# Kernel optimization log

Hardware: AMD Instinct MI355X
Metric: run time of the kernel (lower is better)

Reference implementation:

```python
import jax, jax.numpy as jnp
import numpy as np

N_NODES = 128   # input_series_dim (nodes per graph)
FEAT = 512      # input_series_length
HID = 512       # hidden_channels
OUT = 10        # output_dimension
BATCH = 512     # batch_size


def setup_inputs() -> dict:
    key = jax.random.key(0)
    ks = jax.random.split(key, 9)
    s = 0.02
    x = jax.random.normal(ks[0], (BATCH, N_NODES, FEAT), jnp.float32)
    # dense_to_sparse(ones(N_NODES, N_NODES)) -> fully connected incl. diagonal,
    # row-major order, covering only nodes 0..N_NODES-1 (faithful to source).
    r = jnp.repeat(jnp.arange(N_NODES, dtype=jnp.int32), N_NODES)
    c = jnp.tile(jnp.arange(N_NODES, dtype=jnp.int32), N_NODES)
    edge_index = jnp.stack([r, c])  # (2, N_NODES**2)
    batch = jnp.repeat(jnp.arange(BATCH, dtype=jnp.int32), N_NODES)  # (BATCH*N_NODES,)
    W1 = jax.random.normal(ks[1], (FEAT, HID), jnp.float32) * s
    b1 = jnp.zeros((HID,), jnp.float32)
    W2 = jax.random.normal(ks[2], (HID, HID), jnp.float32) * s
    b2 = jnp.zeros((HID,), jnp.float32)
    W3 = jax.random.normal(ks[3], (HID, HID), jnp.float32) * s
    b3 = jnp.zeros((HID,), jnp.float32)
    Wlin = jax.random.normal(ks[4], (HID, OUT), jnp.float32) * s
    blin = jnp.zeros((OUT,), jnp.float32)
    return {"x": x, "W1": W1, "b1": b1, "W2": W2, "b2": b2, "W3": W3,
            "b3": b3, "Wlin": Wlin, "blin": blin,
            "edge_index": edge_index, "batch": batch}


def gcn_conv(h, src, dst, W, b):
    # PyG GCNConv: linear transform, add self-loops for ALL N nodes, symmetric norm,
    # scatter-add aggregate at dst, add bias.
    N = h.shape[0]
    h = h @ W
    loop = jnp.arange(N, dtype=src.dtype)
    s = jnp.concatenate([src, loop])
    d = jnp.concatenate([dst, loop])
    deg = jax.ops.segment_sum(jnp.ones(s.shape[0], h.dtype), d, num_segments=N)
    dinv = jnp.where(deg > 0, jax.lax.rsqrt(deg), jnp.zeros((), h.dtype))
    norm = dinv[s] * dinv[d]                     # (E+N,)
    out = jax.ops.segment_sum(norm[:, None] * h[s], d, num_segments=N)
    return out + b


def reference(x, W1, b1, W2, b2, W3, b3, Wlin, blin, edge_index, batch):
    x = x.reshape(-1, x.shape[-1]).astype(jnp.float32)   # (B*N_NODES, FEAT)
    src, dst = edge_index[0], edge_index[1]
    h = jax.nn.relu(gcn_conv(x, src, dst, W1, b1))
    h = jax.nn.relu(gcn_conv(h, src, dst, W2, b2))
    h = gcn_conv(h, src, dst, W3, b3)                    # layers == 3 path
    B = BATCH
    sums = jax.ops.segment_sum(h, batch, num_segments=B)
    cnt = jax.ops.segment_sum(jnp.ones((h.shape[0],), h.dtype), batch, num_segments=B)
    pooled = sums / cnt[:, None]                         # global_mean_pool
    # dropout p=0.5 is identity in eval mode
    return pooled @ Wlin + blin                          # (BATCH, OUT)
```

## Files before the change

kernel.cpp:

```cpp
#include <hip/hip_runtime.h>
#include <hip/hip_bf16.h>


typedef __attribute__((ext_vector_type(8))) short short8;
typedef __attribute__((ext_vector_type(4))) float f32x4;
typedef __attribute__((ext_vector_type(2))) unsigned int uint2v;

#define AS_G __attribute__((address_space(1)))
#define AS_L __attribute__((address_space(3)))

__device__ __forceinline__ void gload_lds16(const void* g, void* l) {
  __builtin_amdgcn_global_load_lds((const AS_G void*)g, (AS_L void*)l, 16, 0, 0);
}

__device__ __forceinline__ unsigned int pack2_bf16(float a, float b) {
  unsigned int ua = __float_as_uint(a);
  unsigned int ub = __float_as_uint(b);
  ua += 0x7FFFu + ((ua >> 16) & 1u);
  ub += 0x7FFFu + ((ub >> 16) & 1u);
  return (ua >> 16) | (ub & 0xFFFF0000u);
}

__device__ __forceinline__ unsigned short bf16_rne(float a) {
  unsigned int ua = __float_as_uint(a);
  ua += 0x7FFFu + ((ua >> 16) & 1u);
  return (unsigned short)(ua >> 16);
}

__global__ __launch_bounds__(1024) void fused_gcn(
    const float* __restrict__ x,
    const __hip_bfloat16* __restrict__ W1t,
    const __hip_bfloat16* __restrict__ W2t,
    const float* __restrict__ b1,
    const float* __restrict__ b2,
    float* __restrict__ P)
{
  __shared__ __align__(16) __hip_bfloat16 smem[81920];

  const int t  = threadIdx.x;
  const int g  = blockIdx.x;
  const int wave = t >> 6;
  const int l    = t & 63;
  const int q    = l >> 4;
  const int r16  = l & 15;
  const int wm   = (wave & 1) * 64;
  const int wn   = (wave >> 1) * 64;

  const int arow = t >> 3;
  const int kq   = t & 7;
  const float* ga = x + ((size_t)g * 128 + arow) * 512 + kq * 4;
  const int awoff = arow * 32 + (((kq >> 1) ^ ((arow >> 1) & 3)) << 3) + (kq & 1) * 4;

  const int brow = t >> 2;
  const int bgc  = (t & 3) ^ ((brow >> 1) & 3);
  const size_t boff = (size_t)brow * 512 + bgc * 8;
  const __hip_bfloat16* g1b0 = W1t + boff;
  const __hip_bfloat16* g1b1 = g1b0 + (size_t)256 * 512;

  f32x4 acc[4][4];
#pragma unroll
  for (int i = 0; i < 4; ++i)
#pragma unroll
    for (int j = 0; j < 4; ++j)
      acc[i][j] = (f32x4)0.0f;

  {
    f32x4 a0 = *(const f32x4*)(const void*)ga;
    gload_lds16(g1b0, smem + 49152 + wave * 512);
    gload_lds16(g1b1, smem + 49152 + 8192 + wave * 512);
    uint2v w;
    w[0] = pack2_bf16(a0[0], a0[1]);
    w[1] = pack2_bf16(a0[2], a0[3]);
    *(uint2v*)(void*)(smem + awoff) = w;
  }
  for (int kt = 0; kt < 16; ++kt) {
    const int cur = kt & 1;
    const int nxt = cur ^ 1;
    __syncthreads();

    f32x4 aN;
    if (kt < 15) {
      const int ko = (kt + 1) * 32;
      aN = *(const f32x4*)(const void*)(ga + ko);
      gload_lds16(g1b0 + ko, smem + 49152 + nxt * 16384 + wave * 512);
      gload_lds16(g1b1 + ko, smem + 49152 + nxt * 16384 + 8192 + wave * 512);
    }

    short8 af[4], bfr[4];
#pragma unroll
    for (int i = 0; i < 4; ++i) {
      const int row = wm + i * 16 + r16;
      const int c   = (q ^ ((row >> 1) & 3)) << 3;
      af[i] = *(const short8*)(const void*)(smem + cur * 4096 + row * 32 + c);
    }
#pragma unroll
    for (int j = 0; j < 4; ++j) {
      const int row = wn + j * 16 + r16;
      const int c   = (q ^ ((row >> 1) & 3)) << 3;
      bfr[j] = *(const short8*)(const void*)(smem + 49152 + cur * 16384 + row * 32 + c);
    }
#pragma unroll
    for (int i = 0; i < 4; ++i)
#pragma unroll
      for (int j = 0; j < 4; ++j)
        acc[i][j] = __builtin_amdgcn_mfma_f32_16x16x32_bf16(af[i], bfr[j], acc[i][j], 0, 0, 0);

    if (kt < 15) {
      uint2v w;
      w[0] = pack2_bf16(aN[0], aN[1]);
      w[1] = pack2_bf16(aN[2], aN[3]);
      *(uint2v*)(void*)(smem + nxt * 4096 + awoff) = w;
    }
  }
  __syncthreads();

  float* redf = (float*)(smem + 65536);
  float* Sbuf = (float*)(smem + 67584);

  if (g == 0) {
    float sj[4];
#pragma unroll
    for (int j = 0; j < 4; ++j) {
      float a = 0.0f;
#pragma unroll
      for (int i = 0; i < 4; ++i)
#pragma unroll
        for (int r = 0; r < 4; ++r)
          a += acc[i][j][r];
      a += __shfl_xor(a, 16, 64);
      a += __shfl_xor(a, 32, 64);
      sj[j] = a;
    }
    if (q == 0) {
#pragma unroll
      for (int j = 0; j < 4; ++j) redf[wave * 64 + j * 16 + r16] = sj[j];
    }
    __syncthreads();
    if (t < 512)
      Sbuf[t] = redf[((t >> 6) * 2) * 64 + (t & 63)] +
                redf[((t >> 6) * 2 + 1) * 64 + (t & 63)];
    __syncthreads();
#pragma unroll
    for (int j = 0; j < 4; ++j) {
      const int col = wn + j * 16 + r16;
      const float bv = b1[col];
      const float Sv = Sbuf[col];
#pragma unroll
      for (int i = 0; i < 4; ++i)
#pragma unroll
        for (int r = 0; r < 4; ++r) {
          const int row = wm + i * 16 + q * 4 + r;
          const float v = fmaxf((Sv + acc[i][j][r]) * (1.0f / 129.0f) + bv, 0.0f);
          const float o = __shfl_xor(v, 1, 64);
          if ((r16 & 1) == 0) {
            const int sl = (col >> 3) ^ (row & 7);
            *(unsigned int*)(void*)(smem + row * 512 + sl * 8 + (col & 7)) = pack2_bf16(v, o);
          }
        }
    }
  } else {
#pragma unroll
    for (int j = 0; j < 4; ++j) {
      const int col = wn + j * 16 + r16;
      const float bv = b1[col];
#pragma unroll
      for (int i = 0; i < 4; ++i)
#pragma unroll
        for (int r = 0; r < 4; ++r) {
          const int row = wm + i * 16 + q * 4 + r;
          const float v = fmaxf(acc[i][j][r] + bv, 0.0f);
          const float o = __shfl_xor(v, 1, 64);
          if ((r16 & 1) == 0) {
            const int sl = (col >> 3) ^ (row & 7);
            *(unsigned int*)(void*)(smem + row * 512 + sl * 8 + (col & 7)) = pack2_bf16(v, o);
          }
        }
    }
  }

#pragma unroll
  for (int i = 0; i < 4; ++i)
#pragma unroll
    for (int j = 0; j < 4; ++j)
      acc[i][j] = (f32x4)0.0f;

  const __hip_bfloat16* g2b0 = W2t + boff;
  const __hip_bfloat16* g2b1 = g2b0 + (size_t)256 * 512;

  for (int kt = 0; kt < 16; ++kt) {
    __syncthreads();
    const int ko = kt * 32;
    gload_lds16(g2b0 + ko, smem + 65536 + wave * 512);
    gload_lds16(g2b1 + ko, smem + 65536 + 8192 + wave * 512);
    __syncthreads();

    short8 af[4], bfr[4];
#pragma unroll
    for (int i = 0; i < 4; ++i) {
      const int row = wm + i * 16 + r16;
      const int sl  = (kt * 4 + q) ^ (row & 7);
      af[i] = *(const short8*)(const void*)(smem + row * 512 + sl * 8);
    }
#pragma unroll
    for (int j = 0; j < 4; ++j) {
      const int row = wn + j * 16 + r16;
      const int c   = (q ^ ((row >> 1) & 3)) << 3;
      bfr[j] = *(const short8*)(const void*)(smem + 65536 + row * 32 + c);
    }
#pragma unroll
    for (int i = 0; i < 4; ++i)
#pragma unroll
      for (int j = 0; j < 4; ++j)
        acc[i][j] = __builtin_amdgcn_mfma_f32_16x16x32_bf16(af[i], bfr[j], acc[i][j], 0, 0, 0);
  }
  __syncthreads();

  float pj[4];
  if (g == 0) {
    float sj[4];
#pragma unroll
    for (int j = 0; j < 4; ++j) {
      float a = 0.0f;
#pragma unroll
      for (int i = 0; i < 4; ++i)
#pragma unroll
        for (int r = 0; r < 4; ++r)
          a += acc[i][j][r];
      a += __shfl_xor(a, 16, 64);
      a += __shfl_xor(a, 32, 64);
      sj[j] = a;
    }
    if (q == 0) {
#pragma unroll
      for (int j = 0; j < 4; ++j) redf[wave * 64 + j * 16 + r16] = sj[j];
    }
    __syncthreads();
    if (t < 512)
      Sbuf[t] = redf[((t >> 6) * 2) * 64 + (t & 63)] +
                redf[((t >> 6) * 2 + 1) * 64 + (t & 63)];
    __syncthreads();
#pragma unroll
    for (int j = 0; j < 4; ++j) {
      const float bv = b2[wn + j * 16 + r16];
      const float Sv = Sbuf[wn + j * 16 + r16];
      float a = 0.0f;
#pragma unroll
      for (int i = 0; i < 4; ++i)
#pragma unroll
        for (int r = 0; r < 4; ++r)
          a += fmaxf((Sv + acc[i][j][r]) * (1.0f / 129.0f) + bv, 0.0f);
      a += __shfl_xor(a, 16, 64);
      a += __shfl_xor(a, 32, 64);
      pj[j] = a;
    }
  } else {
#pragma unroll
    for (int j = 0; j < 4; ++j) {
      const float bv = b2[wn + j * 16 + r16];
      float a = 0.0f;
#pragma unroll
      for (int i = 0; i < 4; ++i)
#pragma unroll
        for (int r = 0; r < 4; ++r)
          a += fmaxf(acc[i][j][r] + bv, 0.0f);
      a += __shfl_xor(a, 16, 64);
      a += __shfl_xor(a, 32, 64);
      pj[j] = a;
    }
  }
  if (q == 0) {
#pragma unroll
    for (int j = 0; j < 4; ++j) redf[wave * 64 + j * 16 + r16] = pj[j];
  }
  __syncthreads();
  if (t < 512)
    P[(size_t)g * 512 + t] =
        (redf[((t >> 6) * 2) * 64 + (t & 63)] +
         redf[((t >> 6) * 2 + 1) * 64 + (t & 63)]) * (1.0f / 128.0f);
}

__global__ void fold_w(const float* __restrict__ W3,
                       const float* __restrict__ Wlin,
                       const float* __restrict__ b3,
                       const float* __restrict__ blin,
                       float* __restrict__ Wf, float* __restrict__ bfv) {
  const int c = blockIdx.x;
  const int l = threadIdx.x;
  float acc[10];
#pragma unroll
  for (int o = 0; o < 10; ++o) acc[o] = 0.0f;
  for (int n = l; n < 512; n += 64) {
    const float wv = W3[c * 512 + n];
#pragma unroll
    for (int o = 0; o < 10; ++o) acc[o] += wv * Wlin[n * 10 + o];
  }
#pragma unroll
  for (int off = 32; off; off >>= 1)
#pragma unroll
    for (int o = 0; o < 10; ++o) acc[o] += __shfl_down(acc[o], off, 64);
  if (l == 0) {
#pragma unroll
    for (int o = 0; o < 10; ++o) Wf[c * 10 + o] = acc[o];
  }
  if (c < 10) {
    float s = 0.0f;
    for (int k = l; k < 512; k += 64) s += b3[k] * Wlin[k * 10 + c];
#pragma unroll
    for (int off = 32; off; off >>= 1) s += __shfl_down(s, off, 64);
    if (l == 0) bfv[c] = s + blin[c];
  }
}

__global__ void final_out(const float* __restrict__ P,
                          const float* __restrict__ Wf,
                          const float* __restrict__ bfv,
                          float* __restrict__ out) {
  const int m = blockIdx.x;
  const int l = threadIdx.x;
  float acc[10];
#pragma unroll
  for (int o = 0; o < 10; ++o) acc[o] = 0.0f;
  for (int c = l; c < 512; c += 64) {
    const float p = P[m * 512 + c];
#pragma unroll
    for (int o = 0; o < 10; ++o) acc[o] += p * Wf[c * 10 + o];
  }
#pragma unroll
  for (int off = 32; off; off >>= 1)
#pragma unroll
    for (int o = 0; o < 10; ++o) acc[o] += __shfl_down(acc[o], off, 64);
  if (l == 0) {
#pragma unroll
    for (int o = 0; o < 10; ++o) out[m * 10 + o] = acc[o] + bfv[o];
  }
}

__global__ void transpose512x2(const float* __restrict__ Wa,
                               const float* __restrict__ Wb,
                               unsigned short* __restrict__ Wat,
                               unsigned short* __restrict__ Wbt) {
  const float* W = blockIdx.z ? Wb : Wa;
  unsigned short* Wt = blockIdx.z ? Wbt : Wat;
  __shared__ float tile[32][33];
  const int tx = threadIdx.x, ty = threadIdx.y;
  tile[ty][tx] = W[(blockIdx.y * 32 + ty) * 512 + blockIdx.x * 32 + tx];
  __syncthreads();
  Wt[(blockIdx.x * 32 + ty) * 512 + blockIdx.y * 32 + tx] = bf16_rne(tile[tx][ty]);
}

extern "C" void kernel_launch(void* const* d_in, const int* in_sizes, int n_in,
                              void* d_out, int out_size, void* d_ws, size_t ws_size,
                              hipStream_t stream) {
  const float* x    = (const float*)d_in[0];
  const float* W1   = (const float*)d_in[1];
  const float* b1   = (const float*)d_in[2];
  const float* W2   = (const float*)d_in[3];
  const float* b2   = (const float*)d_in[4];
  const float* W3   = (const float*)d_in[5];
  const float* b3   = (const float*)d_in[6];
  const float* Wlin = (const float*)d_in[7];
  const float* blin = (const float*)d_in[8];
  float* out = (float*)d_out;

  char* ws = (char*)d_ws;
  unsigned short* W1t = (unsigned short*)ws;
  unsigned short* W2t = W1t + 512 * 512;
  float* P            = (float*)(W2t + 512 * 512);
  float* Wf           = P + 512 * 512;
  float* bfv          = Wf + 512 * 10;

  transpose512x2<<<dim3(16, 16, 2), dim3(32, 32), 0, stream>>>(W1, W2, W1t, W2t);
  fold_w<<<512, 64, 0, stream>>>(W3, Wlin, b3, blin, Wf, bfv);

  fused_gcn<<<512, 1024, 0, stream>>>(
      x, (const __hip_bfloat16*)W1t, (const __hip_bfloat16*)W2t, b1, b2, P);

  final_out<<<512, 64, 0, stream>>>(P, Wf, bfv, out);
}
```

Baseline: 287.5 us.

## Load weight B-fragments directly from global into registers, drop LDS staging

Weight fragments for both GEMM layers are now loaded directly from global memory into registers, prefetched one k-step ahead, instead of being staged through LDS with global_load_lds. This removes the B-tile LDS buffers, which shrinks shared memory, and drops the double barrier per k-step in the second layer. Each wave now reads its own weight columns, so the same weight data is fetched by multiple waves via cache. Extra barriers are added around the H1 write and the reduction buffer, which now aliases the A buffer.

```diff
diff --git a/kernel.cpp b/kernel.cpp
--- a/kernel.cpp
+++ b/kernel.cpp
@@ -5,13 +5,6 @@
 typedef __attribute__((ext_vector_type(8))) short short8;
 typedef __attribute__((ext_vector_type(4))) float f32x4;
 typedef __attribute__((ext_vector_type(2))) unsigned int uint2v;
-
-#define AS_G __attribute__((address_space(1)))
-#define AS_L __attribute__((address_space(3)))
-
-__device__ __forceinline__ void gload_lds16(const void* g, void* l) {
-  __builtin_amdgcn_global_load_lds((const AS_G void*)g, (AS_L void*)l, 16, 0, 0);
-}
 
 __device__ __forceinline__ unsigned int pack2_bf16(float a, float b) {
   unsigned int ua = __float_as_uint(a);
@@ -35,7 +28,7 @@
     const float* __restrict__ b2,
     float* __restrict__ P)
 {
-  __shared__ __align__(16) __hip_bfloat16 smem[81920];
+  __shared__ __align__(16) __hip_bfloat16 smem[73728];
 
   const int t  = threadIdx.x;
   const int g  = blockIdx.x;
@@ -46,16 +39,15 @@
   const int wm   = (wave & 1) * 64;
   const int wn   = (wave >> 1) * 64;
 
+  __hip_bfloat16* H1 = smem;
+  __hip_bfloat16* Ab = smem + 65536;
+
   const int arow = t >> 3;
   const int kq   = t & 7;
   const float* ga = x + ((size_t)g * 128 + arow) * 512 + kq * 4;
   const int awoff = arow * 32 + (((kq >> 1) ^ ((arow >> 1) & 3)) << 3) + (kq & 1) * 4;
 
-  const int brow = t >> 2;
-  const int bgc  = (t & 3) ^ ((brow >> 1) & 3);
-  const size_t boff = (size_t)brow * 512 + bgc * 8;
-  const __hip_bfloat16* g1b0 = W1t + boff;
-  const __hip_bfloat16* g1b1 = g1b0 + (size_t)256 * 512;
+  const size_t bfo = (size_t)(wn + r16) * 512 + q * 8;
 
   f32x4 acc[4][4];
 #pragma unroll
@@ -65,57 +57,59 @@
       acc[i][j] = (f32x4)0.0f;
 
   {
-    f32x4 a0 = *(const f32x4*)(const void*)ga;
-    gload_lds16(g1b0, smem + 49152 + wave * 512);
-    gload_lds16(g1b1, smem + 49152 + 8192 + wave * 512);
-    uint2v w;
-    w[0] = pack2_bf16(a0[0], a0[1]);
-    w[1] = pack2_bf16(a0[2], a0[3]);
-    *(uint2v*)(void*)(smem + awoff) = w;
-  }
-  for (int kt = 0; kt < 16; ++kt) {
-    const int cur = kt & 1;
-    const int nxt = cur ^ 1;
-    __syncthreads();
-
-    f32x4 aN;
-    if (kt < 15) {
-      const int ko = (kt + 1) * 32;
-      aN = *(const f32x4*)(const void*)(ga + ko);
-      gload_lds16(g1b0 + ko, smem + 49152 + nxt * 16384 + wave * 512);
-      gload_lds16(g1b1 + ko, smem + 49152 + nxt * 16384 + 8192 + wave * 512);
-    }
-
-    short8 af[4], bfr[4];
-#pragma unroll
-    for (int i = 0; i < 4; ++i) {
-      const int row = wm + i * 16 + r16;
-      const int c   = (q ^ ((row >> 1) & 3)) << 3;
-      af[i] = *(const short8*)(const void*)(smem + cur * 4096 + row * 32 + c);
-    }
-#pragma unroll
-    for (int j = 0; j < 4; ++j) {
-      const int row = wn + j * 16 + r16;
-      const int c   = (q ^ ((row >> 1) & 3)) << 3;
-      bfr[j] = *(const short8*)(const void*)(smem + 49152 + cur * 16384 + row * 32 + c);
-    }
-#pragma unroll
-    for (int i = 0; i < 4; ++i)
-#pragma unroll
-      for (int j = 0; j < 4; ++j)
-        acc[i][j] = __builtin_amdgcn_mfma_f32_16x16x32_bf16(af[i], bfr[j], acc[i][j], 0, 0, 0);
-
-    if (kt < 15) {
+    short8 bcur[4];
+#pragma unroll
+    for (int j = 0; j < 4; ++j)
+      bcur[j] = *(const short8*)(const void*)(W1t + bfo + (size_t)j * 16 * 512);
+    {
+      const f32x4 a0 = *(const f32x4*)(const void*)ga;
       uint2v w;
-      w[0] = pack2_bf16(aN[0], aN[1]);
-      w[1] = pack2_bf16(aN[2], aN[3]);
-      *(uint2v*)(void*)(smem + nxt * 4096 + awoff) = w;
-    }
-  }
-  __syncthreads();
-
-  float* redf = (float*)(smem + 65536);
-  float* Sbuf = (float*)(smem + 67584);
+      w[0] = pack2_bf16(a0[0], a0[1]);
+      w[1] = pack2_bf16(a0[2], a0[3]);
+      *(uint2v*)(void*)(Ab + awoff) = w;
+    }
+    for (int kt = 0; kt < 16; ++kt) {
+      const int cur = kt & 1;
+      const int nxt = cur ^ 1;
+      __syncthreads();
+
+      f32x4 aN;
+      short8 bnxt[4];
+      if (kt < 15) {
+        const int ko = (kt + 1) * 32;
+        aN = *(const f32x4*)(const void*)(ga + ko);
+#pragma unroll
+        for (int j = 0; j < 4; ++j)
+          bnxt[j] = *(const short8*)(const void*)(W1t + bfo + (size_t)j * 16 * 512 + ko);
+      }
+
+      short8 af[4];
+#pragma unroll
+      for (int i = 0; i < 4; ++i) {
+        const int row = wm + i * 16 + r16;
+        const int c   = (q ^ ((row >> 1) & 3)) << 3;
+        af[i] = *(const short8*)(const void*)(Ab + cur * 4096 + row * 32 + c);
+      }
+#pragma unroll
+      for (int i = 0; i < 4; ++i)
+#pragma unroll
+        for (int j = 0; j < 4; ++j)
+          acc[i][j] = __builtin_amdgcn_mfma_f32_16x16x32_bf16(af[i], bcur[j], acc[i][j], 0, 0, 0);
+
+      if (kt < 15) {
+        uint2v w;
+        w[0] = pack2_bf16(aN[0], aN[1]);
+        w[1] = pack2_bf16(aN[2], aN[3]);
+        *(uint2v*)(void*)(Ab + nxt * 4096 + awoff) = w;
+#pragma unroll
+        for (int j = 0; j < 4; ++j) bcur[j] = bnxt[j];
+      }
+    }
+  }
+  __syncthreads();
+
+  float* redf = (float*)(Ab);
+  float* Sbuf = (float*)(Ab + 2048);
 
   if (g == 0) {
     float sj[4];
@@ -154,7 +148,7 @@
           const float o = __shfl_xor(v, 1, 64);
           if ((r16 & 1) == 0) {
             const int sl = (col >> 3) ^ (row & 7);
-            *(unsigned int*)(void*)(smem + row * 512 + sl * 8 + (col & 7)) = pack2_bf16(v, o);
+            *(unsigned int*)(void*)(H1 + row * 512 + sl * 8 + (col & 7)) = pack2_bf16(v, o);
           }
         }
     }
@@ -172,46 +166,46 @@
           const float o = __shfl_xor(v, 1, 64);
           if ((r16 & 1) == 0) {
             const int sl = (col >> 3) ^ (row & 7);
-            *(unsigned int*)(void*)(smem + row * 512 + sl * 8 + (col & 7)) = pack2_bf16(v, o);
+            *(unsigned int*)(void*)(H1 + row * 512 + sl * 8 + (col & 7)) = pack2_bf16(v, o);
           }
         }
     }
   }
+  __syncthreads();
 
 #pragma unroll
   for (int i = 0; i < 4; ++i)
 #pragma unroll
     for (int j = 0; j < 4; ++j)
       acc[i][j] = (f32x4)0.0f;
-
-  const __hip_bfloat16* g2b0 = W2t + boff;
-  const __hip_bfloat16* g2b1 = g2b0 + (size_t)256 * 512;
-
-  for (int kt = 0; kt < 16; ++kt) {
-    __syncthreads();
-    const int ko = kt * 32;
-    gload_lds16(g2b0 + ko, smem + 65536 + wave * 512);
-    gload_lds16(g2b1 + ko, smem + 65536 + 8192 + wave * 512);
-    __syncthreads();
-
-    short8 af[4], bfr[4];
-#pragma unroll
-    for (int i = 0; i < 4; ++i) {
-      const int row = wm + i * 16 + r16;
-      const int sl  = (kt * 4 + q) ^ (row & 7);
-      af[i] = *(const short8*)(const void*)(smem + row * 512 + sl * 8);
-    }
-#pragma unroll
-    for (int j = 0; j < 4; ++j) {
-      const int row = wn + j * 16 + r16;
-      const int c   = (q ^ ((row >> 1) & 3)) << 3;
-      bfr[j] = *(const short8*)(const void*)(smem + 65536 + row * 32 + c);
-    }
-#pragma unroll
-    for (int i = 0; i < 4; ++i)
-#pragma unroll
-      for (int j = 0; j < 4; ++j)
-        acc[i][j] = __builtin_amdgcn_mfma_f32_16x16x32_bf16(af[i], bfr[j], acc[i][j], 0, 0, 0);
+  {
+    short8 bcur[4];
+#pragma unroll
+    for (int j = 0; j < 4; ++j)
+      bcur[j] = *(const short8*)(const void*)(W2t + bfo + (size_t)j * 16 * 512);
+    for (int kt = 0; kt < 16; ++kt) {
+      short8 af[4];
+#pragma unroll
+      for (int i = 0; i < 4; ++i) {
+        const int row = wm + i * 16 + r16;
+        const int sl  = (kt * 4 + q) ^ (row & 7);
+        af[i] = *(const short8*)(const void*)(H1 + row * 512 + sl * 8);
+      }
+      short8 bnxt[4];
+      if (kt < 15) {
+        const int ko = (kt + 1) * 32;
+#pragma unroll
+        for (int j = 0; j < 4; ++j)
+          bnxt[j] = *(const short8*)(const void*)(W2t + bfo + (size_t)j * 16 * 512 + ko);
+      }
+#pragma unroll
+      for (int i = 0; i < 4; ++i)
+#pragma unroll
+        for (int j = 0; j < 4; ++j)
+          acc[i][j] = __builtin_amdgcn_mfma_f32_16x16x32_bf16(af[i], bcur[j], acc[i][j], 0, 0, 0);
+#pragma unroll
+      for (int j = 0; j < 4; ++j) bcur[j] = bnxt[j];
+    }
   }
   __syncthreads();
 
@@ -268,6 +262,7 @@
       pj[j] = a;
     }
   }
+  __syncthreads();
   if (q == 0) {
 #pragma unroll
     for (int j = 0; j < 4; ++j) redf[wave * 64 + j * 16 + r16] = pj[j];
```

Measured after the change: 334.0 us. 16.2% more time.
